# Kernel optimization log

Measured on AMD Instinct MI355X. Metric: run time of the kernel, lower is better.

## Reference

```python
import jax, jax.numpy as jnp
import numpy as np


def setup_inputs() -> dict:
    key = jax.random.key(0)
    ks = jax.random.split(key, 8)
    B, S, Ta, D = 64, 512, 8, 768
    return {
        "memory": jax.random.normal(ks[0], (B, S, D), dtype=jnp.float32),
        "aspect_states": jax.random.normal(ks[1], (B, Ta, D), dtype=jnp.float32),
        "input_ids": jnp.ones((B, S), dtype=jnp.int64),
        "input_t_ids": jnp.ones((B, Ta), dtype=jnp.int64),
        "W1": jax.random.normal(ks[2], (3 * D, D), dtype=jnp.float32) * 0.02,
        "b1": jnp.zeros((D,), dtype=jnp.float32),
        "w2": jax.random.normal(ks[3], (D,), dtype=jnp.float32) * 0.02,
        "Wm": jax.random.normal(ks[4], (D, D), dtype=jnp.float32) * 0.02,
        "bm": jnp.zeros((D,), dtype=jnp.float32),
        "Wd": jax.random.normal(ks[5], (D, 3), dtype=jnp.float32) * 0.02,
        "bd": jnp.zeros((3,), dtype=jnp.float32),
    }


def reference(memory, aspect_states, input_ids, input_t_ids, W1, b1, w2, Wm, bm, Wd, bd):
    B, S, D = memory.shape
    memory_len = jnp.sum(input_ids != 0, axis=-1)          # [B]
    aspect_len = jnp.sum(input_t_ids != 0, axis=-1)        # [B]

    # v_a: mean-pooled aspect representation  [B, D]
    v_a = jnp.sum(aspect_states, axis=1) / aspect_len.astype(memory.dtype)[:, None]
    # v_s: mean-pooled sentence representation [B, D]
    v_s = jnp.sum(memory, axis=1) / memory_len.astype(memory.dtype)[:, None]

    # locationed_memory: memory[i, idx] *= 1 - idx/memory_len[i] for idx < memory_len[i]
    idx = jnp.arange(S, dtype=memory.dtype)                 # [S]
    mlen = memory_len.astype(memory.dtype)[:, None]         # [B, 1]
    loc = jnp.where(idx[None, :] < mlen, 1.0 - idx[None, :] / mlen, 1.0)  # [B, S]
    memory = memory * loc[:, :, None]

    # chunked linear1/linear2 scorer, vectorized:
    # c_t = w2 . tanh(W1 @ [m_t ; v_a ; v_s] + b1)
    W1_m, W1_a, W1_s = W1[:D], W1[D:2 * D], W1[2 * D:]
    ctx = v_a @ W1_a + v_s @ W1_s + b1                      # [B, D]
    h = jnp.tanh(jnp.einsum("bsd,de->bse", memory, W1_m) + ctx[:, None, :])
    scores = h @ w2                                         # [B, S]
    alpha = jax.nn.softmax(scores, axis=1)

    v_ts = jnp.einsum("bsd,bs->bd", memory, alpha)          # [B, D]
    v_ns = v_ts + v_s
    v_ms = jnp.tanh(v_ns @ Wm + bm)
    logits = v_ms @ Wd + bd                                 # [B, 3]
    return logits
```

## Files before the change

### kernel.cpp

```cpp
#include <hip/hip_runtime.h>
#include <hip/hip_bf16.h>


#define NB 64
#define NS 512
#define ND 768
#define NTA 8

typedef __attribute__((ext_vector_type(8))) __bf16 bf16x8;
typedef __attribute__((ext_vector_type(4))) float f32x4;

#define OFF_SCORES 0u
#define OFF_VS 131072u
#define OFF_VTS 327680u
#define OFF_CTX 524288u
#define OFF_U 720896u
#define ZERO_BYTES 917504u
#define OFF_VA 917504u
#define OFF_LENS 1245184u
#define OFF_W1MT 1246208u
#define OFF_MP 2425856u

__device__ __forceinline__ float fast_tanh(float x) {
  x = fminf(fmaxf(x, -15.f), 15.f);
  float t = __expf(2.f * x);
  return __fdividef(t - 1.f, t + 1.f);
}

__device__ __forceinline__ unsigned bfpack2(float a, float b) {
  unsigned ua = __float_as_uint(a), ub = __float_as_uint(b);
  ua = (ua + 0x7FFFu + ((ua >> 16) & 1u)) >> 16;
  ub = (ub + 0x7FFFu + ((ub >> 16) & 1u)) >> 16;
  return ua | (ub << 16);
}

__device__ __forceinline__ unsigned short bf16b(float f) {
  unsigned u = __float_as_uint(f);
  u = (u + 0x7FFFu + ((u >> 16) & 1u)) >> 16;
  return (unsigned short)u;
}

__device__ __forceinline__ void async_copy16(const void* g, void* l) {
  __builtin_amdgcn_global_load_lds(
      (const __attribute__((address_space(1))) void*)g,
      (__attribute__((address_space(3))) void*)l, 16, 0, 0);
}

__global__ __launch_bounds__(256) void k_pre(const float* __restrict__ W1,
                                             unsigned short* __restrict__ w1mt,
                                             const int* __restrict__ ids,
                                             const int* __restrict__ tids,
                                             const float* __restrict__ aspect,
                                             float* __restrict__ v_a,
                                             float* __restrict__ lens) {
  int bid = blockIdx.x, tid = threadIdx.x;
  if (bid < 576) {
    __shared__ float tile[32][33];
    int bx = bid % 24, by = bid / 24;
    int tx = tid & 31, ty = tid >> 5;
    for (int j = 0; j < 32; j += 8)
      tile[ty + j][tx] = W1[(size_t)(by * 32 + ty + j) * ND + bx * 32 + tx];
    __syncthreads();
    for (int j = 0; j < 32; j += 8)
      w1mt[(size_t)(bx * 32 + ty + j) * ND + by * 32 + tx] = bf16b(tile[tx][ty + j]);
  } else {
    int b = bid - 576;
    __shared__ int red[256];
    __shared__ float sh_inva;
    int cnt = 0;
    for (int j = tid; j < NS; j += 256) cnt += (ids[b * NS + j] != 0);
    red[tid] = cnt;
    __syncthreads();
    for (int s = 128; s > 0; s >>= 1) {
      if (tid < s) red[tid] += red[tid + s];
      __syncthreads();
    }
    if (tid == 0) {
      int mlen = red[0];
      int acnt = 0;
      for (int t = 0; t < NTA; ++t) acnt += (tids[b * NTA + t] != 0);
      lens[b] = (float)mlen;
      lens[64 + b] = 1.0f / (float)mlen;
      float inva = 1.0f / (float)acnt;
      lens[128 + b] = inva;
      sh_inva = inva;
    }
    __syncthreads();
    float inva = sh_inva;
    for (int j = tid; j < ND; j += 256) {
      float s = 0.f;
      for (int t = 0; t < NTA; ++t) s += aspect[((size_t)b * NTA + t) * ND + j];
      v_a[b * ND + j] = s * inva;
    }
  }
}

__global__ __launch_bounds__(192) void k_vs_mprime(const float* __restrict__ memory,
                                                   const float* __restrict__ lens,
                                                   float* __restrict__ v_s,
                                                   unsigned short* __restrict__ mp) {
  int sc = blockIdx.x, b = blockIdx.y, tid = threadIdx.x;
  int d0 = tid * 4;
  float inv_mlen = lens[64 + b];
  float mlenf = lens[b];
  float s0 = 0, s1 = 0, s2 = 0, s3 = 0;
  for (int s = 0; s < 32; ++s) {
    int srow = sc * 32 + s;
    size_t row = (size_t)b * NS + srow;
    const float4 v = *(const float4*)(memory + row * ND + d0);
    s0 += v.x; s1 += v.y; s2 += v.z; s3 += v.w;
    float fs = (float)srow;
    float loc = (fs < mlenf) ? 1.0f - fs * inv_mlen : 1.0f;
    uint2 pk;
    pk.x = bfpack2(v.x * loc, v.y * loc);
    pk.y = bfpack2(v.z * loc, v.w * loc);
    *(uint2*)(mp + row * ND + d0) = pk;
  }
  float* p = v_s + b * ND + d0;
  atomicAdd(p + 0, s0 * inv_mlen);
  atomicAdd(p + 1, s1 * inv_mlen);
  atomicAdd(p + 2, s2 * inv_mlen);
  atomicAdd(p + 3, s3 * inv_mlen);
}

__global__ __launch_bounds__(128) void k_ctx(const float* __restrict__ W1,
                                             const float* __restrict__ v_a,
                                             const float* __restrict__ v_s,
                                             float* __restrict__ ctx) {
  int et = blockIdx.x, b = blockIdx.y, dc = blockIdx.z, tid = threadIdx.x;
  __shared__ float vbuf[384];
  for (int j = tid; j < 384; j += 128) {
    int k = dc * 384 + j;
    vbuf[j] = (k < ND) ? v_a[b * ND + k] : v_s[b * ND + (k - ND)];
  }
  __syncthreads();
  int e = et * 128 + tid;
  float acc = 0.f;
  const float* Wk = W1 + (size_t)(ND + dc * 384) * ND + e;
#pragma unroll 8
  for (int j = 0; j < 384; ++j) acc += vbuf[j] * Wk[(size_t)j * ND];
  atomicAdd(&ctx[b * ND + e], acc);
}

__global__ __launch_bounds__(256, 2) void k_gemm_scores(const unsigned short* __restrict__ mp,
                                                        const unsigned short* __restrict__ w1mt,
                                                        const float* __restrict__ ctx,
                                                        const float* __restrict__ b1,
                                                        const float* __restrict__ w2,
                                                        float* __restrict__ scores) {
  __shared__ char lds[49152];
  char* ldsA = lds;
  char* ldsB = lds + 32768;
  const int tid = threadIdx.x;
  const int wave = tid >> 6, lane = tid & 63;
  const int et = blockIdx.x, rt = blockIdx.y;
  const int row0 = rt * 256, n0 = et * 128;
  const int b = row0 >> 9;
  const int wm = wave & 1, wn = wave >> 1;

  const int lrow = lane >> 3;
  const int qlog = (lane & 7) ^ lrow;
  const char* Abase = (const char*)mp + (size_t)(row0 + lrow) * (ND * 2) + qlog * 16;
  const char* Bbase = (const char*)w1mt + (size_t)(n0 + lrow) * (ND * 2) + qlog * 16;

  f32x4 acc[8][4];
#pragma unroll
  for (int i = 0; i < 8; ++i)
#pragma unroll
    for (int t = 0; t < 4; ++t) acc[i][t] = (f32x4){0.f, 0.f, 0.f, 0.f};

  const int q2 = lane >> 4, c = lane & 15;
  int offA0[8], offB0[4];
#pragma unroll
  for (int i = 0; i < 8; ++i) {
    int ml = wm * 128 + i * 16 + c;
    offA0[i] = ml * 128 + ((q2 ^ (ml & 7)) * 16);
  }
#pragma unroll
  for (int t = 0; t < 4; ++t) {
    int nl = wn * 64 + t * 16 + c;
    offB0[t] = nl * 128 + ((q2 ^ (nl & 7)) * 16);
  }

  for (int kb = 0; kb < ND * 2; kb += 128) {
#pragma unroll
    for (int i = 0; i < 8; ++i) {
      int g = wave * 8 + i;
      async_copy16(Abase + (size_t)g * 8 * (ND * 2) + kb, ldsA + g * 1024);
    }
#pragma unroll
    for (int i = 0; i < 4; ++i) {
      int g = wave * 4 + i;
      async_copy16(Bbase + (size_t)g * 8 * (ND * 2) + kb, ldsB + g * 1024);
    }
    __syncthreads();
#pragma unroll
    for (int kk = 0; kk < 2; ++kk) {
      const int x = kk * 64;
      bf16x8 bfrag[4];
#pragma unroll
      for (int t = 0; t < 4; ++t) bfrag[t] = *(const bf16x8*)(ldsB + (offB0[t] ^ x));
#pragma unroll
      for (int i = 0; i < 8; ++i) {
        bf16x8 afrag = *(const bf16x8*)(ldsA + (offA0[i] ^ x));
#pragma unroll
        for (int t = 0; t < 4; ++t)
          acc[i][t] = __builtin_amdgcn_mfma_f32_16x16x32_bf16(afrag, bfrag[t], acc[i][t], 0, 0, 0);
      }
    }
    __syncthreads();
  }

  float ctxv[4], w2v[4];
#pragma unroll
  for (int t = 0; t < 4; ++t) {
    int n = n0 + wn * 64 + t * 16 + c;
    ctxv[t] = ctx[b * ND + n] + b1[n];
    w2v[t] = w2[n];
  }
#pragma unroll
  for (int i = 0; i < 8; ++i) {
#pragma unroll
    for (int r = 0; r < 4; ++r) {
      float s = 0.f;
#pragma unroll
      for (int t = 0; t < 4; ++t) s += fast_tanh(acc[i][t][r] + ctxv[t]) * w2v[t];
      s += __shfl_xor(s, 1, 64);
      s += __shfl_xor(s, 2, 64);
      s += __shfl_xor(s, 4, 64);
      s += __shfl_xor(s, 8, 64);
      if (c == 0) atomicAdd(&scores[row0 + wm * 128 + i * 16 + q2 * 4 + r], s);
    }
  }
}

__global__ __launch_bounds__(192) void k_vts_sm(const unsigned short* __restrict__ mp,
                                                const float* __restrict__ scores,
                                                float* __restrict__ v_ts) {
  int sc = blockIdx.x, b = blockIdx.y, tid = threadIdx.x;
  int wid = tid >> 6, lane = tid & 63;
  __shared__ float sm[3], ss[3];
  __shared__ float al[32];
  float v[3];
#pragma unroll
  for (int k = 0; k < 3; ++k) {
    int j = tid + k * 192;
    v[k] = (j < NS) ? scores[b * NS + j] : -1e30f;
  }
  float m = fmaxf(fmaxf(v[0], v[1]), v[2]);
  for (int off = 1; off < 64; off <<= 1) m = fmaxf(m, __shfl_xor(m, off, 64));
  if (lane == 0) sm[wid] = m;
  __syncthreads();
  float M = fmaxf(fmaxf(sm[0], sm[1]), sm[2]);
  float e = 0.f;
#pragma unroll
  for (int k = 0; k < 3; ++k)
    if (tid + k * 192 < NS) e += __expf(v[k] - M);
  for (int off = 1; off < 64; off <<= 1) e += __shfl_xor(e, off, 64);
  if (lane == 0) ss[wid] = e;
  __syncthreads();
  float invS = 1.0f / (ss[0] + ss[1] + ss[2]);
  if (tid < 32) al[tid] = __expf(scores[b * NS + sc * 32 + tid] - M) * invS;
  __syncthreads();

  int d0 = tid * 4;
  float a0 = 0, a1 = 0, a2 = 0, a3 = 0;
  for (int s = 0; s < 32; ++s) {
    size_t row = (size_t)b * NS + sc * 32 + s;
    uint2 pk = *(const uint2*)(mp + row * ND + d0);
    float a = al[s];
    a0 += a * __uint_as_float(pk.x << 16);
    a1 += a * __uint_as_float(pk.x & 0xFFFF0000u);
    a2 += a * __uint_as_float(pk.y << 16);
    a3 += a * __uint_as_float(pk.y & 0xFFFF0000u);
  }
  float* p = v_ts + b * ND + d0;
  atomicAdd(p + 0, a0);
  atomicAdd(p + 1, a1);
  atomicAdd(p + 2, a2);
  atomicAdd(p + 3, a3);
}

__global__ __launch_bounds__(128) void k_final1(const float* __restrict__ v_ts,
                                                const float* __restrict__ v_s,
                                                const float* __restrict__ Wm,
                                                float* __restrict__ u) {
  int et = blockIdx.x, b = blockIdx.y, dc = blockIdx.z, tid = threadIdx.x;
  __shared__ float vbuf[192];
  for (int j = tid; j < 192; j += 128) {
    int d = dc * 192 + j;
    vbuf[j] = v_ts[b * ND + d] + v_s[b * ND + d];
  }
  __syncthreads();
  int e = et * 128 + tid;
  float acc = 0.f;
  const float* Wk = Wm + (size_t)(dc * 192) * ND + e;
#pragma unroll 8
  for (int j = 0; j < 192; ++j) acc += vbuf[j] * Wk[(size_t)j * ND];
  atomicAdd(&u[b * ND + e], acc);
}

__global__ __launch_bounds__(256) void k_final2(const float* __restrict__ u,
                                                const float* __restrict__ bm,
                                                const float* __restrict__ Wd,
                                                const float* __restrict__ bd,
                                                float* __restrict__ out) {
  int b = blockIdx.x, tid = threadIdx.x;
  int wid = tid >> 6, lane = tid & 63;
  __shared__ float red[4][3];
  float p0 = 0, p1 = 0, p2 = 0;
  for (int e = tid; e < ND; e += 256) {
    float vm = fast_tanh(u[b * ND + e] + bm[e]);
    p0 += vm * Wd[e * 3 + 0];
    p1 += vm * Wd[e * 3 + 1];
    p2 += vm * Wd[e * 3 + 2];
  }
  for (int off = 1; off < 64; off <<= 1) {
    p0 += __shfl_xor(p0, off, 64);
    p1 += __shfl_xor(p1, off, 64);
    p2 += __shfl_xor(p2, off, 64);
  }
  if (lane == 0) { red[wid][0] = p0; red[wid][1] = p1; red[wid][2] = p2; }
  __syncthreads();
  if (tid == 0) {
    out[b * 3 + 0] = red[0][0] + red[1][0] + red[2][0] + red[3][0] + bd[0];
    out[b * 3 + 1] = red[0][1] + red[1][1] + red[2][1] + red[3][1] + bd[1];
    out[b * 3 + 2] = red[0][2] + red[1][2] + red[2][2] + red[3][2] + bd[2];
  }
}

extern "C" void kernel_launch(void* const* d_in, const int* in_sizes, int n_in,
                              void* d_out, int out_size, void* d_ws, size_t ws_size,
                              hipStream_t stream) {
  const float* memory = (const float*)d_in[0];
  const float* aspect = (const float*)d_in[1];
  const int* ids = (const int*)d_in[2];
  const int* tids = (const int*)d_in[3];
  const float* W1 = (const float*)d_in[4];
  const float* b1 = (const float*)d_in[5];
  const float* w2 = (const float*)d_in[6];
  const float* Wm = (const float*)d_in[7];
  const float* bm = (const float*)d_in[8];
  const float* Wd = (const float*)d_in[9];
  const float* bd = (const float*)d_in[10];
  float* out = (float*)d_out;

  char* ws = (char*)d_ws;
  float* scores = (float*)(ws + OFF_SCORES);
  float* v_s = (float*)(ws + OFF_VS);
  float* v_ts = (float*)(ws + OFF_VTS);
  float* ctx = (float*)(ws + OFF_CTX);
  float* u = (float*)(ws + OFF_U);
  float* v_a = (float*)(ws + OFF_VA);
  float* lens = (float*)(ws + OFF_LENS);
  unsigned short* w1mt = (unsigned short*)(ws + OFF_W1MT);
  unsigned short* mp = (unsigned short*)(ws + OFF_MP);

  hipMemsetAsync(ws, 0, ZERO_BYTES, stream);

  k_pre<<<640, 256, 0, stream>>>(W1, w1mt, ids, tids, aspect, v_a, lens);
  k_vs_mprime<<<dim3(16, NB), 192, 0, stream>>>(memory, lens, v_s, mp);
  k_ctx<<<dim3(6, NB, 4), 128, 0, stream>>>(W1, v_a, v_s, ctx);
  k_gemm_scores<<<dim3(6, 128), 256, 0, stream>>>(mp, w1mt, ctx, b1, w2, scores);
  k_vts_sm<<<dim3(16, NB), 192, 0, stream>>>(mp, scores, v_ts);
  k_final1<<<dim3(6, NB, 4), 128, 0, stream>>>(v_ts, v_s, Wm, u);
  k_final2<<<NB, 256, 0, stream>>>(u, bm, Wd, bd, out);
}
```

Before: 325.9 us.

## Batch GEMV weight reuse, shrink GEMM tiles with XCD mapping, fold memset into prep

The ctx and final1 GEMVs now process 8 batch rows per block, so each weight load is reused across 8 batches instead of one, which cuts redundant weight traffic. The score GEMM tile goes from 256 to 128 rows with smaller LDS, giving more blocks and higher occupancy, and block ids are remapped so neighbouring row tiles land on the same XCD for cache locality. The workspace memset is folded into extra blocks of the prep kernel to save one launch. Smaller GEMM tiles lower the data reuse per block, and the zeroing now depends on the prep kernel running first.

Measured after the change: 324.6 us. No clear change (-0.4%).

```diff
diff --git a/kernel.cpp b/kernel.cpp
--- a/kernel.cpp
+++ b/kernel.cpp
@@ -52,7 +52,8 @@
                                              const int* __restrict__ tids,
                                              const float* __restrict__ aspect,
                                              float* __restrict__ v_a,
-                                             float* __restrict__ lens) {
+                                             float* __restrict__ lens,
+                                             char* __restrict__ zws) {
   int bid = blockIdx.x, tid = threadIdx.x;
   if (bid < 576) {
     __shared__ float tile[32][33];
@@ -63,7 +64,7 @@
     __syncthreads();
     for (int j = 0; j < 32; j += 8)
       w1mt[(size_t)(bx * 32 + ty + j) * ND + by * 32 + tx] = bf16b(tile[tx][ty + j]);
-  } else {
+  } else if (bid < 640) {
     int b = bid - 576;
     __shared__ int red[256];
     __shared__ float sh_inva;
@@ -92,6 +93,9 @@
       for (int t = 0; t < NTA; ++t) s += aspect[((size_t)b * NTA + t) * ND + j];
       v_a[b * ND + j] = s * inva;
     }
+  } else {
+    uint4 z = {0u, 0u, 0u, 0u};
+    *(uint4*)(zws + (size_t)(bid - 640) * 4096 + tid * 16) = z;
   }
 }
 
@@ -123,38 +127,48 @@
   atomicAdd(p + 3, s3 * inv_mlen);
 }
 
-__global__ __launch_bounds__(128) void k_ctx(const float* __restrict__ W1,
+__global__ __launch_bounds__(256) void k_ctx(const float* __restrict__ W1,
                                              const float* __restrict__ v_a,
                                              const float* __restrict__ v_s,
                                              float* __restrict__ ctx) {
-  int et = blockIdx.x, b = blockIdx.y, dc = blockIdx.z, tid = threadIdx.x;
-  __shared__ float vbuf[384];
-  for (int j = tid; j < 384; j += 128) {
-    int k = dc * 384 + j;
-    vbuf[j] = (k < ND) ? v_a[b * ND + k] : v_s[b * ND + (k - ND)];
-  }
-  __syncthreads();
-  int e = et * 128 + tid;
-  float acc = 0.f;
-  const float* Wk = W1 + (size_t)(ND + dc * 384) * ND + e;
-#pragma unroll 8
-  for (int j = 0; j < 384; ++j) acc += vbuf[j] * Wk[(size_t)j * ND];
-  atomicAdd(&ctx[b * ND + e], acc);
-}
-
-__global__ __launch_bounds__(256, 2) void k_gemm_scores(const unsigned short* __restrict__ mp,
-                                                        const unsigned short* __restrict__ w1mt,
-                                                        const float* __restrict__ ctx,
-                                                        const float* __restrict__ b1,
-                                                        const float* __restrict__ w2,
-                                                        float* __restrict__ scores) {
-  __shared__ char lds[49152];
+  int et = blockIdx.x, bt = blockIdx.y, dc = blockIdx.z, tid = threadIdx.x;
+  __shared__ float vbuf[8][192];
+  int b0 = bt * 8;
+  for (int l = tid; l < 8 * 192; l += 256) {
+    int bb = l / 192, jj = l % 192;
+    int k = dc * 192 + jj;
+    vbuf[bb][jj] = (k < ND) ? v_a[(b0 + bb) * ND + k] : v_s[(b0 + bb) * ND + (k - ND)];
+  }
+  __syncthreads();
+  int e = et * 256 + tid;
+  const float* Wk = W1 + (size_t)(ND + dc * 192) * ND + e;
+  float acc[8] = {0.f, 0.f, 0.f, 0.f, 0.f, 0.f, 0.f, 0.f};
+#pragma unroll 4
+  for (int j = 0; j < 192; ++j) {
+    float w = Wk[(size_t)j * ND];
+#pragma unroll
+    for (int bb = 0; bb < 8; ++bb) acc[bb] += vbuf[bb][j] * w;
+  }
+#pragma unroll
+  for (int bb = 0; bb < 8; ++bb) atomicAdd(&ctx[(b0 + bb) * ND + e], acc[bb]);
+}
+
+__global__ __launch_bounds__(256) void k_gemm_scores(const unsigned short* __restrict__ mp,
+                                                     const unsigned short* __restrict__ w1mt,
+                                                     const float* __restrict__ ctx,
+                                                     const float* __restrict__ b1,
+                                                     const float* __restrict__ w2,
+                                                     float* __restrict__ scores) {
+  __shared__ char lds[32768];
   char* ldsA = lds;
-  char* ldsB = lds + 32768;
+  char* ldsB = lds + 16384;
   const int tid = threadIdx.x;
   const int wave = tid >> 6, lane = tid & 63;
-  const int et = blockIdx.x, rt = blockIdx.y;
-  const int row0 = rt * 256, n0 = et * 128;
+  const int bid = blockIdx.x;
+  const int xcd = bid & 7, j = bid >> 3;
+  const int et = j % 6;
+  const int rt = xcd * 32 + j / 6;
+  const int row0 = rt * 128, n0 = et * 128;
   const int b = row0 >> 9;
   const int wm = wave & 1, wn = wave >> 1;
 
@@ -163,34 +177,27 @@
   const char* Abase = (const char*)mp + (size_t)(row0 + lrow) * (ND * 2) + qlog * 16;
   const char* Bbase = (const char*)w1mt + (size_t)(n0 + lrow) * (ND * 2) + qlog * 16;
 
-  f32x4 acc[8][4];
-#pragma unroll
-  for (int i = 0; i < 8; ++i)
+  f32x4 acc[4][4];
+#pragma unroll
+  for (int i = 0; i < 4; ++i)
 #pragma unroll
     for (int t = 0; t < 4; ++t) acc[i][t] = (f32x4){0.f, 0.f, 0.f, 0.f};
 
   const int q2 = lane >> 4, c = lane & 15;
-  int offA0[8], offB0[4];
-#pragma unroll
-  for (int i = 0; i < 8; ++i) {
-    int ml = wm * 128 + i * 16 + c;
+  int offA0[4], offB0[4];
+#pragma unroll
+  for (int i = 0; i < 4; ++i) {
+    int ml = wm * 64 + i * 16 + c;
     offA0[i] = ml * 128 + ((q2 ^ (ml & 7)) * 16);
-  }
-#pragma unroll
-  for (int t = 0; t < 4; ++t) {
-    int nl = wn * 64 + t * 16 + c;
-    offB0[t] = nl * 128 + ((q2 ^ (nl & 7)) * 16);
+    int nl = wn * 64 + i * 16 + c;
+    offB0[i] = nl * 128 + ((q2 ^ (nl & 7)) * 16);
   }
 
   for (int kb = 0; kb < ND * 2; kb += 128) {
-#pragma unroll
-    for (int i = 0; i < 8; ++i) {
-      int g = wave * 8 + i;
-      async_copy16(Abase + (size_t)g * 8 * (ND * 2) + kb, ldsA + g * 1024);
-    }
 #pragma unroll
     for (int i = 0; i < 4; ++i) {
       int g = wave * 4 + i;
+      async_copy16(Abase + (size_t)g * 8 * (ND * 2) + kb, ldsA + g * 1024);
       async_copy16(Bbase + (size_t)g * 8 * (ND * 2) + kb, ldsB + g * 1024);
     }
     __syncthreads();
@@ -201,7 +208,7 @@
 #pragma unroll
       for (int t = 0; t < 4; ++t) bfrag[t] = *(const bf16x8*)(ldsB + (offB0[t] ^ x));
 #pragma unroll
-      for (int i = 0; i < 8; ++i) {
+      for (int i = 0; i < 4; ++i) {
         bf16x8 afrag = *(const bf16x8*)(ldsA + (offA0[i] ^ x));
 #pragma unroll
         for (int t = 0; t < 4; ++t)
@@ -219,7 +226,7 @@
     w2v[t] = w2[n];
   }
 #pragma unroll
-  for (int i = 0; i < 8; ++i) {
+  for (int i = 0; i < 4; ++i) {
 #pragma unroll
     for (int r = 0; r < 4; ++r) {
       float s = 0.f;
@@ -229,7 +236,7 @@
       s += __shfl_xor(s, 2, 64);
       s += __shfl_xor(s, 4, 64);
       s += __shfl_xor(s, 8, 64);
-      if (c == 0) atomicAdd(&scores[row0 + wm * 128 + i * 16 + q2 * 4 + r], s);
+      if (c == 0) atomicAdd(&scores[row0 + wm * 64 + i * 16 + q2 * 4 + r], s);
     }
   }
 }
@@ -281,23 +288,30 @@
   atomicAdd(p + 3, a3);
 }
 
-__global__ __launch_bounds__(128) void k_final1(const float* __restrict__ v_ts,
+__global__ __launch_bounds__(256) void k_final1(const float* __restrict__ v_ts,
                                                 const float* __restrict__ v_s,
                                                 const float* __restrict__ Wm,
                                                 float* __restrict__ u) {
-  int et = blockIdx.x, b = blockIdx.y, dc = blockIdx.z, tid = threadIdx.x;
-  __shared__ float vbuf[192];
-  for (int j = tid; j < 192; j += 128) {
-    int d = dc * 192 + j;
-    vbuf[j] = v_ts[b * ND + d] + v_s[b * ND + d];
-  }
-  __syncthreads();
-  int e = et * 128 + tid;
-  float acc = 0.f;
+  int et = blockIdx.x, bt = blockIdx.y, dc = blockIdx.z, tid = threadIdx.x;
+  __shared__ float vbuf[8][192];
+  int b0 = bt * 8;
+  for (int l = tid; l < 8 * 192; l += 256) {
+    int bb = l / 192, jj = l % 192;
+    int d = dc * 192 + jj;
+    vbuf[bb][jj] = v_ts[(b0 + bb) * ND + d] + v_s[(b0 + bb) * ND + d];
+  }
+  __syncthreads();
+  int e = et * 256 + tid;
   const float* Wk = Wm + (size_t)(dc * 192) * ND + e;
-#pragma unroll 8
-  for (int j = 0; j < 192; ++j) acc += vbuf[j] * Wk[(size_t)j * ND];
-  atomicAdd(&u[b * ND + e], acc);
+  float acc[8] = {0.f, 0.f, 0.f, 0.f, 0.f, 0.f, 0.f, 0.f};
+#pragma unroll 4
+  for (int j = 0; j < 192; ++j) {
+    float w = Wk[(size_t)j * ND];
+#pragma unroll
+    for (int bb = 0; bb < 8; ++bb) acc[bb] += vbuf[bb][j] * w;
+  }
+#pragma unroll
+  for (int bb = 0; bb < 8; ++bb) atomicAdd(&u[(b0 + bb) * ND + e], acc[bb]);
 }
 
 __global__ __launch_bounds__(256) void k_final2(const float* __restrict__ u,
@@ -356,13 +370,11 @@
   unsigned short* w1mt = (unsigned short*)(ws + OFF_W1MT);
   unsigned short* mp = (unsigned short*)(ws + OFF_MP);
 
-  hipMemsetAsync(ws, 0, ZERO_BYTES, stream);
-
-  k_pre<<<640, 256, 0, stream>>>(W1, w1mt, ids, tids, aspect, v_a, lens);
+  k_pre<<<864, 256, 0, stream>>>(W1, w1mt, ids, tids, aspect, v_a, lens, ws);
   k_vs_mprime<<<dim3(16, NB), 192, 0, stream>>>(memory, lens, v_s, mp);
-  k_ctx<<<dim3(6, NB, 4), 128, 0, stream>>>(W1, v_a, v_s, ctx);
-  k_gemm_scores<<<dim3(6, 128), 256, 0, stream>>>(mp, w1mt, ctx, b1, w2, scores);
+  k_ctx<<<dim3(3, 8, 8), 256, 0, stream>>>(W1, v_a, v_s, ctx);
+  k_gemm_scores<<<1536, 256, 0, stream>>>(mp, w1mt, ctx, b1, w2, scores);
   k_vts_sm<<<dim3(16, NB), 192, 0, stream>>>(mp, scores, v_ts);
-  k_final1<<<dim3(6, NB, 4), 128, 0, stream>>>(v_ts, v_s, Wm, u);
+  k_final1<<<dim3(3, 8, 4), 256, 0, stream>>>(v_ts, v_s, Wm, u);
   k_final2<<<NB, 256, 0, stream>>>(u, bm, Wd, bd, out);
 }
```
